# Kernel optimization log

Hardware: AMD Instinct MI355X
Metric: run time of the kernel (lower is better)

## Reference

```python
import jax, jax.numpy as jnp
import numpy as np

B, N, DIM, NUM_NODE = 512, 64, 128, 43098
ALPHA = 0.2          # LeakyReLU negative slope (opt.alpha)
NEG_INF = -9e15      # mask value used by LocalAggregator


def setup_inputs() -> dict:
    key = jax.random.key(0)
    ks = jax.random.split(key, 6)
    stdv = 1.0 / np.sqrt(DIM)
    inputs = jax.random.randint(ks[0], (B, N), 0, NUM_NODE)
    adj = jax.random.randint(ks[1], (B, N, N), 0, 5)          # edge types 0..4
    mask_item = jax.random.randint(ks[2], (B, N), 0, 2)
    item = jax.random.randint(ks[3], (B, N), 0, NUM_NODE)
    embedding = jax.random.uniform(ks[4], (NUM_NODE, DIM), minval=-stdv, maxval=stdv, dtype=jnp.float32)
    attn_a = jax.random.uniform(ks[5], (4, DIM), minval=-stdv, maxval=stdv, dtype=jnp.float32)  # a_0..a_3
    return dict(inputs=inputs, adj=adj, mask_item=mask_item, item=item,
                embedding=embedding, attn_a=attn_a)


def _local_agg(h, adj, attn_a):
    # GCE-GNN LocalAggregator: a_input[b,i,j,:] = h[b,i,:]*h[b,j,:];
    # e_k[b,i,j] = leakyrelu(a_input @ a_k). Computed without materializing
    # the [B,N,N,D] tensor: e_k = leakyrelu(einsum over d of h_i*h_j*a_k).
    e = jax.nn.leaky_relu(jnp.einsum('kd,bid,bjd->kbij', attn_a, h, h), ALPHA)  # [4,B,N,N]
    alpha = jnp.full(e.shape[1:], NEG_INF, dtype=e.dtype)
    for k in range(4):  # edge-type masked selection: adj==k+1 -> e_k
        alpha = jnp.where(adj == k + 1, e[k], alpha)
    alpha = jax.nn.softmax(alpha, axis=-1)          # [B,N,N]
    return jnp.einsum('bij,bjd->bid', alpha, h)     # [B,N,D]


def reference(inputs, adj, mask_item, item, embedding, attn_a):
    h = embedding[inputs]                 # [B,N,D] embedding gather
    h_local = _local_agg(h, adj, attn_a)  # GAT-style local aggregation
    # F.dropout with training=False (eval/inference) is identity
    return h_local
```

## Files before the change

### kernel.cpp

```cpp
#include <hip/hip_runtime.h>
#include <hip/hip_bf16.h>


#define LRELU    0.2f

typedef __bf16 bf16x8 __attribute__((ext_vector_type(8)));
typedef float  f32x4  __attribute__((ext_vector_type(4)));

union FragU { bf16x8 v; unsigned u[4]; uint4 q; };

__device__ __forceinline__ unsigned pk2(float lo, float hi) {
  __hip_bfloat162 t = __float22bfloat162_rn(float2{lo, hi});
  unsigned u;
  __builtin_memcpy(&u, &t, 4);
  return u;
}
__device__ __forceinline__ float bflo(unsigned u) { return __builtin_bit_cast(float, u << 16); }
__device__ __forceinline__ float bfhi(unsigned u) { return __builtin_bit_cast(float, u & 0xffff0000u); }

__global__ __launch_bounds__(512, 4)
void cg_kernel(const int* __restrict__ inputs, const int* __restrict__ adj,
               const float* __restrict__ embedding, const float* __restrict__ attn_a,
               float* __restrict__ out) {
  __shared__ unsigned short Hb[64 * 128];
  __shared__ unsigned short HbT[128 * 64];
  __shared__ unsigned short Pl[64 * 64];
  __shared__ float aaL[512];
  __shared__ float redS[64 * 2];

  const int b   = blockIdx.x;
  const int tid = threadIdx.x;
  const int w   = tid >> 6;
  const int l   = tid & 63;
  const int lr  = l & 15;
  const int lg  = l >> 4;
  const int it  = w >> 1;
  const int jh  = w & 1;

  char* HbB  = (char*)Hb;
  char* HbTB = (char*)HbT;
  char* PlB  = (char*)Pl;

  const int row = tid >> 3;
  const int c   = tid & 7;
  const int idx = inputs[b * 64 + row];

  int adjv[2][4];
#pragma unroll
  for (int jt2 = 0; jt2 < 2; ++jt2)
#pragma unroll
    for (int r = 0; r < 4; ++r)
      adjv[jt2][r] = adj[b * 4096 + (16 * it + 4 * lg + r) * 64 + 32 * jh + 16 * jt2 + lr];

  const float4* src = (const float4*)(embedding + (long)idx * 128 + c * 16);
  float4 v0 = src[0], v1 = src[1], v2 = src[2], v3 = src[3];
  aaL[tid] = attn_a[tid];

  unsigned pk[8];
  pk[0] = pk2(v0.x, v0.y); pk[1] = pk2(v0.z, v0.w);
  pk[2] = pk2(v1.x, v1.y); pk[3] = pk2(v1.z, v1.w);
  pk[4] = pk2(v2.x, v2.y); pk[5] = pk2(v2.z, v2.w);
  pk[6] = pk2(v3.x, v3.y); pk[7] = pk2(v3.z, v3.w);
  const int rswz = (row & 7) << 4;
  *(uint4*)(HbB + ((row * 256 + c * 32)      ^ rswz)) = uint4{pk[0], pk[1], pk[2], pk[3]};
  *(uint4*)(HbB + ((row * 256 + c * 32 + 16) ^ rswz)) = uint4{pk[4], pk[5], pk[6], pk[7]};
#pragma unroll
  for (int s = 0; s < 16; ++s) {
    int e = (s + 3 * c) & 15;
    int d = c * 16 + e;
    unsigned short hv = (unsigned short)((e & 1) ? (pk[e >> 1] >> 16) : (pk[e >> 1] & 0xffffu));
    *(unsigned short*)(HbTB + ((d * 128 + row * 2) ^ ((d & 7) << 4))) = hv;
  }
  __syncthreads();

  f32x4 acc[4][2];
#pragma unroll
  for (int k = 0; k < 4; ++k)
#pragma unroll
    for (int jt2 = 0; jt2 < 2; ++jt2) acc[k][jt2] = f32x4{0.f, 0.f, 0.f, 0.f};

  const int arow = 16 * it + lr;
  const int aswz = (lr & 7) << 4;

#pragma unroll
  for (int kc = 0; kc < 4; ++kc) {
    const int dsl = kc * 32 + lg * 8;
    uint4 ha = *(const uint4*)(HbB + ((arow * 256 + dsl * 2) ^ aswz));
    float hfa[8];
    hfa[0] = bflo(ha.x); hfa[1] = bfhi(ha.x);
    hfa[2] = bflo(ha.y); hfa[3] = bfhi(ha.y);
    hfa[4] = bflo(ha.z); hfa[5] = bfhi(ha.z);
    hfa[6] = bflo(ha.w); hfa[7] = bfhi(ha.w);
    FragU bf0, bf1;
    {
      int jr0 = 16 * (2 * jh) + lr;
      int jr1 = 16 * (2 * jh + 1) + lr;
      bf0.q = *(const uint4*)(HbB + ((jr0 * 256 + dsl * 2) ^ aswz));
      bf1.q = *(const uint4*)(HbB + ((jr1 * 256 + dsl * 2) ^ aswz));
    }
#pragma unroll
    for (int k = 0; k < 4; ++k) {
      float4 a0 = *(const float4*)&aaL[k * 128 + dsl];
      float4 a1 = *(const float4*)&aaL[k * 128 + dsl + 4];
      FragU afr;
      afr.u[0] = pk2(hfa[0] * a0.x, hfa[1] * a0.y);
      afr.u[1] = pk2(hfa[2] * a0.z, hfa[3] * a0.w);
      afr.u[2] = pk2(hfa[4] * a1.x, hfa[5] * a1.y);
      afr.u[3] = pk2(hfa[6] * a1.z, hfa[7] * a1.w);
      acc[k][0] = __builtin_amdgcn_mfma_f32_16x16x32_bf16(afr.v, bf0.v, acc[k][0], 0, 0, 0);
      acc[k][1] = __builtin_amdgcn_mfma_f32_16x16x32_bf16(afr.v, bf1.v, acc[k][1], 0, 0, 0);
    }
  }

  float p[2][4];
#pragma unroll
  for (int jt2 = 0; jt2 < 2; ++jt2)
#pragma unroll
    for (int r = 0; r < 4; ++r) {
      int av = adjv[jt2][r];
      float s = acc[0][jt2][r];
      s = (av == 2) ? acc[1][jt2][r] : s;
      s = (av == 3) ? acc[2][jt2][r] : s;
      s = (av == 4) ? acc[3][jt2][r] : s;
      float sl = s > 0.f ? s : LRELU * s;
      p[jt2][r] = (av != 0) ? __expf(sl) : 0.f;
    }
#pragma unroll
  for (int r = 0; r < 4; ++r) {
    int i = 16 * it + 4 * lg + r;
    int iswz = (i & 7) << 4;
    *(unsigned short*)(PlB + ((i * 128 + (32 * jh + lr) * 2)      ^ iswz)) = (unsigned short)(pk2(p[0][r], p[0][r]) & 0xffffu);
    *(unsigned short*)(PlB + ((i * 128 + (32 * jh + 16 + lr) * 2) ^ iswz)) = (unsigned short)(pk2(p[1][r], p[1][r]) & 0xffffu);
    float ss = p[0][r] + p[1][r];
    ss += __shfl_xor(ss, 1);
    ss += __shfl_xor(ss, 2);
    ss += __shfl_xor(ss, 4);
    ss += __shfl_xor(ss, 8);
    if (lr == 0) redS[i * 2 + jh] = ss;
  }
  __syncthreads();
  float z4[4];
#pragma unroll
  for (int r = 0; r < 4; ++r) {
    int i = 16 * it + 4 * lg + r;
    z4[r] = redS[i * 2] + redS[i * 2 + 1];
  }

  FragU afrP[2];
#pragma unroll
  for (int kc2 = 0; kc2 < 2; ++kc2) {
    int prow = 16 * it + lr;
    afrP[kc2].q = *(const uint4*)(PlB + ((prow * 128 + (kc2 * 32 + lg * 8) * 2) ^ aswz));
  }
  f32x4 pv[4];
#pragma unroll
  for (int dtl = 0; dtl < 4; ++dtl) pv[dtl] = f32x4{0.f, 0.f, 0.f, 0.f};
#pragma unroll
  for (int dtl = 0; dtl < 4; ++dtl) {
#pragma unroll
    for (int kc2 = 0; kc2 < 2; ++kc2) {
      int drow = 64 * jh + 16 * dtl + lr;
      FragU bfr;
      bfr.q = *(const uint4*)(HbTB + ((drow * 128 + (kc2 * 32 + lg * 8) * 2) ^ ((drow & 7) << 4)));
      pv[dtl] = __builtin_amdgcn_mfma_f32_16x16x32_bf16(afrP[kc2].v, bfr.v, pv[dtl], 0, 0, 0);
    }
  }

#pragma unroll
  for (int r = 0; r < 4; ++r) {
    int i = 16 * it + 4 * lg + r;
    float invz = 1.0f / z4[r];
#pragma unroll
    for (int dtl = 0; dtl < 4; ++dtl) {
      int d = 64 * jh + 16 * dtl + lr;
      out[(b * 64 + i) * 128 + d] = pv[dtl][r] * invz;
    }
  }
}

extern "C" void kernel_launch(void* const* d_in, const int* in_sizes, int n_in,
                              void* d_out, int out_size, void* d_ws, size_t ws_size,
                              hipStream_t stream) {
  (void)in_sizes; (void)n_in; (void)d_ws; (void)ws_size; (void)out_size;
  const int*   inputs    = (const int*)d_in[0];
  const int*   adj       = (const int*)d_in[1];
  const float* embedding = (const float*)d_in[4];
  const float* attn_a    = (const float*)d_in[5];
  float*       out       = (float*)d_out;
  cg_kernel<<<dim3(512), dim3(512), 0, stream>>>(inputs, adj, embedding, attn_a, out);
}
```

Baseline: 18.72 us.

## Split each batch across two 256-thread blocks by query-row halves

Each batch is now handled by two blocks of 256 threads, and each block computes 32 of the 64 query rows. Both blocks still gather and convert the full 64x128 embedding tile, plus its transpose, into shared memory, so that gather work is done twice. The aim is to double the grid to 1024 blocks for better occupancy and load balance across CUs, and to shrink per-block shared memory for the P and reduction buffers. The cost is redundant embedding loads and transposes, and more work per thread during staging.

```diff
diff --git a/kernel.cpp b/kernel.cpp
--- a/kernel.cpp
+++ b/kernel.cpp
@@ -18,17 +18,19 @@
 __device__ __forceinline__ float bflo(unsigned u) { return __builtin_bit_cast(float, u << 16); }
 __device__ __forceinline__ float bfhi(unsigned u) { return __builtin_bit_cast(float, u & 0xffff0000u); }
 
-__global__ __launch_bounds__(512, 4)
+__global__ __launch_bounds__(256, 4)
 void cg_kernel(const int* __restrict__ inputs, const int* __restrict__ adj,
                const float* __restrict__ embedding, const float* __restrict__ attn_a,
                float* __restrict__ out) {
   __shared__ unsigned short Hb[64 * 128];
   __shared__ unsigned short HbT[128 * 64];
-  __shared__ unsigned short Pl[64 * 64];
+  __shared__ unsigned short Pl[32 * 64];
   __shared__ float aaL[512];
-  __shared__ float redS[64 * 2];
-
-  const int b   = blockIdx.x;
+  __shared__ float redS[32 * 2];
+
+  const int bid = blockIdx.x;
+  const int b   = bid >> 1;
+  const int bi  = bid & 1;
   const int tid = threadIdx.x;
   const int w   = tid >> 6;
   const int l   = tid & 63;
@@ -41,33 +43,42 @@
   char* HbTB = (char*)HbT;
   char* PlB  = (char*)Pl;
 
-  const int row = tid >> 3;
-  const int c   = tid & 7;
+  const int row = tid >> 2;
+  const int c   = tid & 3;
   const int idx = inputs[b * 64 + row];
 
   int adjv[2][4];
 #pragma unroll
   for (int jt2 = 0; jt2 < 2; ++jt2)
 #pragma unroll
-    for (int r = 0; r < 4; ++r)
-      adjv[jt2][r] = adj[b * 4096 + (16 * it + 4 * lg + r) * 64 + 32 * jh + 16 * jt2 + lr];
-
-  const float4* src = (const float4*)(embedding + (long)idx * 128 + c * 16);
-  float4 v0 = src[0], v1 = src[1], v2 = src[2], v3 = src[3];
+    for (int r = 0; r < 4; ++r) {
+      int iloc = 16 * it + 4 * lg + r;
+      adjv[jt2][r] = adj[b * 4096 + (32 * bi + iloc) * 64 + 32 * jh + 16 * jt2 + lr];
+    }
+
+  const float4* src = (const float4*)(embedding + (long)idx * 128 + c * 32);
+  float4 v[8];
+#pragma unroll
+  for (int q = 0; q < 8; ++q) v[q] = src[q];
   aaL[tid] = attn_a[tid];
-
-  unsigned pk[8];
-  pk[0] = pk2(v0.x, v0.y); pk[1] = pk2(v0.z, v0.w);
-  pk[2] = pk2(v1.x, v1.y); pk[3] = pk2(v1.z, v1.w);
-  pk[4] = pk2(v2.x, v2.y); pk[5] = pk2(v2.z, v2.w);
-  pk[6] = pk2(v3.x, v3.y); pk[7] = pk2(v3.z, v3.w);
+  aaL[tid + 256] = attn_a[tid + 256];
+
+  unsigned pk[16];
+#pragma unroll
+  for (int q = 0; q < 8; ++q) {
+    pk[2 * q]     = pk2(v[q].x, v[q].y);
+    pk[2 * q + 1] = pk2(v[q].z, v[q].w);
+  }
   const int rswz = (row & 7) << 4;
-  *(uint4*)(HbB + ((row * 256 + c * 32)      ^ rswz)) = uint4{pk[0], pk[1], pk[2], pk[3]};
-  *(uint4*)(HbB + ((row * 256 + c * 32 + 16) ^ rswz)) = uint4{pk[4], pk[5], pk[6], pk[7]};
-#pragma unroll
-  for (int s = 0; s < 16; ++s) {
-    int e = (s + 3 * c) & 15;
-    int d = c * 16 + e;
+  const int base = row * 256 + c * 64;
+  *(uint4*)(HbB + ((base)      ^ rswz)) = uint4{pk[0],  pk[1],  pk[2],  pk[3]};
+  *(uint4*)(HbB + ((base + 16) ^ rswz)) = uint4{pk[4],  pk[5],  pk[6],  pk[7]};
+  *(uint4*)(HbB + ((base + 32) ^ rswz)) = uint4{pk[8],  pk[9],  pk[10], pk[11]};
+  *(uint4*)(HbB + ((base + 48) ^ rswz)) = uint4{pk[12], pk[13], pk[14], pk[15]};
+#pragma unroll
+  for (int s = 0; s < 32; ++s) {
+    int e = (s + 2 * c) & 31;
+    int d = c * 32 + e;
     unsigned short hv = (unsigned short)((e & 1) ? (pk[e >> 1] >> 16) : (pk[e >> 1] & 0xffffu));
     *(unsigned short*)(HbTB + ((d * 128 + row * 2) ^ ((d & 7) << 4))) = hv;
   }
@@ -79,7 +90,7 @@
 #pragma unroll
     for (int jt2 = 0; jt2 < 2; ++jt2) acc[k][jt2] = f32x4{0.f, 0.f, 0.f, 0.f};
 
-  const int arow = 16 * it + lr;
+  const int arow = 32 * bi + 16 * it + lr;
   const int aswz = (lr & 7) << 4;
 
 #pragma unroll
@@ -93,8 +104,8 @@
     hfa[6] = bflo(ha.w); hfa[7] = bfhi(ha.w);
     FragU bf0, bf1;
     {
-      int jr0 = 16 * (2 * jh) + lr;
-      int jr1 = 16 * (2 * jh + 1) + lr;
+      int jr0 = 32 * jh + lr;
+      int jr1 = 32 * jh + 16 + lr;
       bf0.q = *(const uint4*)(HbB + ((jr0 * 256 + dsl * 2) ^ aswz));
       bf1.q = *(const uint4*)(HbB + ((jr1 * 256 + dsl * 2) ^ aswz));
     }
@@ -127,23 +138,23 @@
     }
 #pragma unroll
   for (int r = 0; r < 4; ++r) {
-    int i = 16 * it + 4 * lg + r;
-    int iswz = (i & 7) << 4;
-    *(unsigned short*)(PlB + ((i * 128 + (32 * jh + lr) * 2)      ^ iswz)) = (unsigned short)(pk2(p[0][r], p[0][r]) & 0xffffu);
-    *(unsigned short*)(PlB + ((i * 128 + (32 * jh + 16 + lr) * 2) ^ iswz)) = (unsigned short)(pk2(p[1][r], p[1][r]) & 0xffffu);
+    int iloc = 16 * it + 4 * lg + r;
+    int iswz = (iloc & 7) << 4;
+    *(unsigned short*)(PlB + ((iloc * 128 + (32 * jh + lr) * 2)      ^ iswz)) = (unsigned short)(pk2(p[0][r], p[0][r]) & 0xffffu);
+    *(unsigned short*)(PlB + ((iloc * 128 + (32 * jh + 16 + lr) * 2) ^ iswz)) = (unsigned short)(pk2(p[1][r], p[1][r]) & 0xffffu);
     float ss = p[0][r] + p[1][r];
     ss += __shfl_xor(ss, 1);
     ss += __shfl_xor(ss, 2);
     ss += __shfl_xor(ss, 4);
     ss += __shfl_xor(ss, 8);
-    if (lr == 0) redS[i * 2 + jh] = ss;
+    if (lr == 0) redS[iloc * 2 + jh] = ss;
   }
   __syncthreads();
   float z4[4];
 #pragma unroll
   for (int r = 0; r < 4; ++r) {
-    int i = 16 * it + 4 * lg + r;
-    z4[r] = redS[i * 2] + redS[i * 2 + 1];
+    int iloc = 16 * it + 4 * lg + r;
+    z4[r] = redS[iloc * 2] + redS[iloc * 2 + 1];
   }
 
   FragU afrP[2];
@@ -168,12 +179,12 @@
 
 #pragma unroll
   for (int r = 0; r < 4; ++r) {
-    int i = 16 * it + 4 * lg + r;
+    int iloc = 16 * it + 4 * lg + r;
     float invz = 1.0f / z4[r];
 #pragma unroll
     for (int dtl = 0; dtl < 4; ++dtl) {
       int d = 64 * jh + 16 * dtl + lr;
-      out[(b * 64 + i) * 128 + d] = pv[dtl][r] * invz;
+      out[(b * 64 + 32 * bi + iloc) * 128 + d] = pv[dtl][r] * invz;
     }
   }
 }
@@ -187,5 +198,5 @@
   const float* embedding = (const float*)d_in[4];
   const float* attn_a    = (const float*)d_in[5];
   float*       out       = (float*)d_out;
-  cg_kernel<<<dim3(512), dim3(512), 0, stream>>>(inputs, adj, embedding, attn_a, out);
+  cg_kernel<<<dim3(1024), dim3(256), 0, stream>>>(inputs, adj, embedding, attn_a, out);
 }
```

New measurement: 25.05 us. 1.34x slower.

## Process two batches per block and prefetch the second batch's gather during compute

Applied to the files above, without the earlier changes.

Each block now handles two batch elements. The embedding gather and adjacency loads for the second batch are issued before computing the first, so their global-memory latency overlaps the first batch's MFMA work. The grid is halved to 256 blocks and the launch bound occupancy hint drops to 2. On a 256-CU device this leaves roughly one block per CU and serializes two batches per block, so overlap gains may be offset by lost parallelism and higher register pressure.

```diff
diff --git a/kernel.cpp b/kernel.cpp
--- a/kernel.cpp
+++ b/kernel.cpp
@@ -18,7 +18,7 @@
 __device__ __forceinline__ float bflo(unsigned u) { return __builtin_bit_cast(float, u << 16); }
 __device__ __forceinline__ float bfhi(unsigned u) { return __builtin_bit_cast(float, u & 0xffff0000u); }
 
-__global__ __launch_bounds__(512, 4)
+__global__ __launch_bounds__(512, 2)
 void cg_kernel(const int* __restrict__ inputs, const int* __restrict__ adj,
                const float* __restrict__ embedding, const float* __restrict__ attn_a,
                float* __restrict__ out) {
@@ -28,7 +28,7 @@
   __shared__ float aaL[512];
   __shared__ float redS[64 * 2];
 
-  const int b   = blockIdx.x;
+  const int bid = blockIdx.x;
   const int tid = threadIdx.x;
   const int w   = tid >> 6;
   const int l   = tid & 63;
@@ -41,141 +41,167 @@
   char* HbTB = (char*)HbT;
   char* PlB  = (char*)Pl;
 
-  const int row = tid >> 3;
-  const int c   = tid & 7;
-  const int idx = inputs[b * 64 + row];
-
-  int adjv[2][4];
+  const int row  = tid >> 3;
+  const int c    = tid & 7;
+  const int rswz = (row & 7) << 4;
+  const int aswz = (lr & 7) << 4;
+
+  aaL[tid] = attn_a[tid];
+
+  auto stage = [&](const float4& v0, const float4& v1, const float4& v2, const float4& v3) {
+    unsigned pk[8];
+    pk[0] = pk2(v0.x, v0.y); pk[1] = pk2(v0.z, v0.w);
+    pk[2] = pk2(v1.x, v1.y); pk[3] = pk2(v1.z, v1.w);
+    pk[4] = pk2(v2.x, v2.y); pk[5] = pk2(v2.z, v2.w);
+    pk[6] = pk2(v3.x, v3.y); pk[7] = pk2(v3.z, v3.w);
+    *(uint4*)(HbB + ((row * 256 + c * 32)      ^ rswz)) = uint4{pk[0], pk[1], pk[2], pk[3]};
+    *(uint4*)(HbB + ((row * 256 + c * 32 + 16) ^ rswz)) = uint4{pk[4], pk[5], pk[6], pk[7]};
+#pragma unroll
+    for (int s = 0; s < 16; ++s) {
+      int e = (s + 3 * c) & 15;
+      int d = c * 16 + e;
+      unsigned short hv = (unsigned short)((e & 1) ? (pk[e >> 1] >> 16) : (pk[e >> 1] & 0xffffu));
+      *(unsigned short*)(HbTB + ((d * 128 + row * 2) ^ ((d & 7) << 4))) = hv;
+    }
+  };
+
+  auto compute = [&](int b, const int (&adjv)[2][4]) {
+    f32x4 acc[4][2];
+#pragma unroll
+    for (int k = 0; k < 4; ++k)
+#pragma unroll
+      for (int jt2 = 0; jt2 < 2; ++jt2) acc[k][jt2] = f32x4{0.f, 0.f, 0.f, 0.f};
+
+    const int arow = 16 * it + lr;
+#pragma unroll
+    for (int kc = 0; kc < 4; ++kc) {
+      const int dsl = kc * 32 + lg * 8;
+      uint4 ha = *(const uint4*)(HbB + ((arow * 256 + dsl * 2) ^ aswz));
+      float hfa[8];
+      hfa[0] = bflo(ha.x); hfa[1] = bfhi(ha.x);
+      hfa[2] = bflo(ha.y); hfa[3] = bfhi(ha.y);
+      hfa[4] = bflo(ha.z); hfa[5] = bfhi(ha.z);
+      hfa[6] = bflo(ha.w); hfa[7] = bfhi(ha.w);
+      FragU bf0, bf1;
+      {
+        int jr0 = 32 * jh + lr;
+        int jr1 = 32 * jh + 16 + lr;
+        bf0.q = *(const uint4*)(HbB + ((jr0 * 256 + dsl * 2) ^ aswz));
+        bf1.q = *(const uint4*)(HbB + ((jr1 * 256 + dsl * 2) ^ aswz));
+      }
+#pragma unroll
+      for (int k = 0; k < 4; ++k) {
+        float4 a0 = *(const float4*)&aaL[k * 128 + dsl];
+        float4 a1 = *(const float4*)&aaL[k * 128 + dsl + 4];
+        FragU afr;
+        afr.u[0] = pk2(hfa[0] * a0.x, hfa[1] * a0.y);
+        afr.u[1] = pk2(hfa[2] * a0.z, hfa[3] * a0.w);
+        afr.u[2] = pk2(hfa[4] * a1.x, hfa[5] * a1.y);
+        afr.u[3] = pk2(hfa[6] * a1.z, hfa[7] * a1.w);
+        acc[k][0] = __builtin_amdgcn_mfma_f32_16x16x32_bf16(afr.v, bf0.v, acc[k][0], 0, 0, 0);
+        acc[k][1] = __builtin_amdgcn_mfma_f32_16x16x32_bf16(afr.v, bf1.v, acc[k][1], 0, 0, 0);
+      }
+    }
+
+    float p[2][4];
+#pragma unroll
+    for (int jt2 = 0; jt2 < 2; ++jt2)
+#pragma unroll
+      for (int r = 0; r < 4; ++r) {
+        int av = adjv[jt2][r];
+        float s = acc[0][jt2][r];
+        s = (av == 2) ? acc[1][jt2][r] : s;
+        s = (av == 3) ? acc[2][jt2][r] : s;
+        s = (av == 4) ? acc[3][jt2][r] : s;
+        float sl = s > 0.f ? s : LRELU * s;
+        p[jt2][r] = (av != 0) ? __expf(sl) : 0.f;
+      }
+#pragma unroll
+    for (int r = 0; r < 4; ++r) {
+      int i = 16 * it + 4 * lg + r;
+      int iswz = (i & 7) << 4;
+      *(unsigned short*)(PlB + ((i * 128 + (32 * jh + lr) * 2)      ^ iswz)) = (unsigned short)(pk2(p[0][r], p[0][r]) & 0xffffu);
+      *(unsigned short*)(PlB + ((i * 128 + (32 * jh + 16 + lr) * 2) ^ iswz)) = (unsigned short)(pk2(p[1][r], p[1][r]) & 0xffffu);
+      float ss = p[0][r] + p[1][r];
+      ss += __shfl_xor(ss, 1);
+      ss += __shfl_xor(ss, 2);
+      ss += __shfl_xor(ss, 4);
+      ss += __shfl_xor(ss, 8);
+      if (lr == 0) redS[i * 2 + jh] = ss;
+    }
+    __syncthreads();
+    float z4[4];
+#pragma unroll
+    for (int r = 0; r < 4; ++r) {
+      int i = 16 * it + 4 * lg + r;
+      z4[r] = redS[i * 2] + redS[i * 2 + 1];
+    }
+
+    FragU afrP[2];
+#pragma unroll
+    for (int kc2 = 0; kc2 < 2; ++kc2) {
+      int prow = 16 * it + lr;
+      afrP[kc2].q = *(const uint4*)(PlB + ((prow * 128 + (kc2 * 32 + lg * 8) * 2) ^ aswz));
+    }
+    f32x4 pv[4];
+#pragma unroll
+    for (int dtl = 0; dtl < 4; ++dtl) pv[dtl] = f32x4{0.f, 0.f, 0.f, 0.f};
+#pragma unroll
+    for (int dtl = 0; dtl < 4; ++dtl) {
+#pragma unroll
+      for (int kc2 = 0; kc2 < 2; ++kc2) {
+        int drow = 64 * jh + 16 * dtl + lr;
+        FragU bfr;
+        bfr.q = *(const uint4*)(HbTB + ((drow * 128 + (kc2 * 32 + lg * 8) * 2) ^ ((drow & 7) << 4)));
+        pv[dtl] = __builtin_amdgcn_mfma_f32_16x16x32_bf16(afrP[kc2].v, bfr.v, pv[dtl], 0, 0, 0);
+      }
+    }
+#pragma unroll
+    for (int r = 0; r < 4; ++r) {
+      int i = 16 * it + 4 * lg + r;
+      float invz = 1.0f / z4[r];
+#pragma unroll
+      for (int dtl = 0; dtl < 4; ++dtl) {
+        int d = 64 * jh + 16 * dtl + lr;
+        out[(b * 64 + i) * 128 + d] = pv[dtl][r] * invz;
+      }
+    }
+  };
+
+  const int bA = 2 * bid;
+  const int bB = 2 * bid + 1;
+
+  int adjA[2][4];
 #pragma unroll
   for (int jt2 = 0; jt2 < 2; ++jt2)
 #pragma unroll
     for (int r = 0; r < 4; ++r)
-      adjv[jt2][r] = adj[b * 4096 + (16 * it + 4 * lg + r) * 64 + 32 * jh + 16 * jt2 + lr];
-
-  const float4* src = (const float4*)(embedding + (long)idx * 128 + c * 16);
-  float4 v0 = src[0], v1 = src[1], v2 = src[2], v3 = src[3];
-  aaL[tid] = attn_a[tid];
-
-  unsigned pk[8];
-  pk[0] = pk2(v0.x, v0.y); pk[1] = pk2(v0.z, v0.w);
-  pk[2] = pk2(v1.x, v1.y); pk[3] = pk2(v1.z, v1.w);
-  pk[4] = pk2(v2.x, v2.y); pk[5] = pk2(v2.z, v2.w);
-  pk[6] = pk2(v3.x, v3.y); pk[7] = pk2(v3.z, v3.w);
-  const int rswz = (row & 7) << 4;
-  *(uint4*)(HbB + ((row * 256 + c * 32)      ^ rswz)) = uint4{pk[0], pk[1], pk[2], pk[3]};
-  *(uint4*)(HbB + ((row * 256 + c * 32 + 16) ^ rswz)) = uint4{pk[4], pk[5], pk[6], pk[7]};
-#pragma unroll
-  for (int s = 0; s < 16; ++s) {
-    int e = (s + 3 * c) & 15;
-    int d = c * 16 + e;
-    unsigned short hv = (unsigned short)((e & 1) ? (pk[e >> 1] >> 16) : (pk[e >> 1] & 0xffffu));
-    *(unsigned short*)(HbTB + ((d * 128 + row * 2) ^ ((d & 7) << 4))) = hv;
+      adjA[jt2][r] = adj[bA * 4096 + (16 * it + 4 * lg + r) * 64 + 32 * jh + 16 * jt2 + lr];
+  {
+    const int idxA = inputs[bA * 64 + row];
+    const float4* srcA = (const float4*)(embedding + (long)idxA * 128 + c * 16);
+    float4 a0 = srcA[0], a1 = srcA[1], a2 = srcA[2], a3 = srcA[3];
+    stage(a0, a1, a2, a3);
   }
   __syncthreads();
 
-  f32x4 acc[4][2];
-#pragma unroll
-  for (int k = 0; k < 4; ++k)
-#pragma unroll
-    for (int jt2 = 0; jt2 < 2; ++jt2) acc[k][jt2] = f32x4{0.f, 0.f, 0.f, 0.f};
-
-  const int arow = 16 * it + lr;
-  const int aswz = (lr & 7) << 4;
-
-#pragma unroll
-  for (int kc = 0; kc < 4; ++kc) {
-    const int dsl = kc * 32 + lg * 8;
-    uint4 ha = *(const uint4*)(HbB + ((arow * 256 + dsl * 2) ^ aswz));
-    float hfa[8];
-    hfa[0] = bflo(ha.x); hfa[1] = bfhi(ha.x);
-    hfa[2] = bflo(ha.y); hfa[3] = bfhi(ha.y);
-    hfa[4] = bflo(ha.z); hfa[5] = bfhi(ha.z);
-    hfa[6] = bflo(ha.w); hfa[7] = bfhi(ha.w);
-    FragU bf0, bf1;
-    {
-      int jr0 = 16 * (2 * jh) + lr;
-      int jr1 = 16 * (2 * jh + 1) + lr;
-      bf0.q = *(const uint4*)(HbB + ((jr0 * 256 + dsl * 2) ^ aswz));
-      bf1.q = *(const uint4*)(HbB + ((jr1 * 256 + dsl * 2) ^ aswz));
-    }
-#pragma unroll
-    for (int k = 0; k < 4; ++k) {
-      float4 a0 = *(const float4*)&aaL[k * 128 + dsl];
-      float4 a1 = *(const float4*)&aaL[k * 128 + dsl + 4];
-      FragU afr;
-      afr.u[0] = pk2(hfa[0] * a0.x, hfa[1] * a0.y);
-      afr.u[1] = pk2(hfa[2] * a0.z, hfa[3] * a0.w);
-      afr.u[2] = pk2(hfa[4] * a1.x, hfa[5] * a1.y);
-      afr.u[3] = pk2(hfa[6] * a1.z, hfa[7] * a1.w);
-      acc[k][0] = __builtin_amdgcn_mfma_f32_16x16x32_bf16(afr.v, bf0.v, acc[k][0], 0, 0, 0);
-      acc[k][1] = __builtin_amdgcn_mfma_f32_16x16x32_bf16(afr.v, bf1.v, acc[k][1], 0, 0, 0);
-    }
-  }
-
-  float p[2][4];
+  const int idxB = inputs[bB * 64 + row];
+  const float4* srcB = (const float4*)(embedding + (long)idxB * 128 + c * 16);
+  float4 b0 = srcB[0], b1 = srcB[1], b2 = srcB[2], b3 = srcB[3];
+  int adjB[2][4];
 #pragma unroll
   for (int jt2 = 0; jt2 < 2; ++jt2)
 #pragma unroll
-    for (int r = 0; r < 4; ++r) {
-      int av = adjv[jt2][r];
-      float s = acc[0][jt2][r];
-      s = (av == 2) ? acc[1][jt2][r] : s;
-      s = (av == 3) ? acc[2][jt2][r] : s;
-      s = (av == 4) ? acc[3][jt2][r] : s;
-      float sl = s > 0.f ? s : LRELU * s;
-      p[jt2][r] = (av != 0) ? __expf(sl) : 0.f;
-    }
-#pragma unroll
-  for (int r = 0; r < 4; ++r) {
-    int i = 16 * it + 4 * lg + r;
-    int iswz = (i & 7) << 4;
-    *(unsigned short*)(PlB + ((i * 128 + (32 * jh + lr) * 2)      ^ iswz)) = (unsigned short)(pk2(p[0][r], p[0][r]) & 0xffffu);
-    *(unsigned short*)(PlB + ((i * 128 + (32 * jh + 16 + lr) * 2) ^ iswz)) = (unsigned short)(pk2(p[1][r], p[1][r]) & 0xffffu);
-    float ss = p[0][r] + p[1][r];
-    ss += __shfl_xor(ss, 1);
-    ss += __shfl_xor(ss, 2);
-    ss += __shfl_xor(ss, 4);
-    ss += __shfl_xor(ss, 8);
-    if (lr == 0) redS[i * 2 + jh] = ss;
-  }
+    for (int r = 0; r < 4; ++r)
+      adjB[jt2][r] = adj[bB * 4096 + (16 * it + 4 * lg + r) * 64 + 32 * jh + 16 * jt2 + lr];
+
+  compute(bA, adjA);
+
   __syncthreads();
-  float z4[4];
-#pragma unroll
-  for (int r = 0; r < 4; ++r) {
-    int i = 16 * it + 4 * lg + r;
-    z4[r] = redS[i * 2] + redS[i * 2 + 1];
-  }
-
-  FragU afrP[2];
-#pragma unroll
-  for (int kc2 = 0; kc2 < 2; ++kc2) {
-    int prow = 16 * it + lr;
-    afrP[kc2].q = *(const uint4*)(PlB + ((prow * 128 + (kc2 * 32 + lg * 8) * 2) ^ aswz));
-  }
-  f32x4 pv[4];
-#pragma unroll
-  for (int dtl = 0; dtl < 4; ++dtl) pv[dtl] = f32x4{0.f, 0.f, 0.f, 0.f};
-#pragma unroll
-  for (int dtl = 0; dtl < 4; ++dtl) {
-#pragma unroll
-    for (int kc2 = 0; kc2 < 2; ++kc2) {
-      int drow = 64 * jh + 16 * dtl + lr;
-      FragU bfr;
-      bfr.q = *(const uint4*)(HbTB + ((drow * 128 + (kc2 * 32 + lg * 8) * 2) ^ ((drow & 7) << 4)));
-      pv[dtl] = __builtin_amdgcn_mfma_f32_16x16x32_bf16(afrP[kc2].v, bfr.v, pv[dtl], 0, 0, 0);
-    }
-  }
-
-#pragma unroll
-  for (int r = 0; r < 4; ++r) {
-    int i = 16 * it + 4 * lg + r;
-    float invz = 1.0f / z4[r];
-#pragma unroll
-    for (int dtl = 0; dtl < 4; ++dtl) {
-      int d = 64 * jh + 16 * dtl + lr;
-      out[(b * 64 + i) * 128 + d] = pv[dtl][r] * invz;
-    }
-  }
+  stage(b0, b1, b2, b3);
+  __syncthreads();
+
+  compute(bB, adjB);
 }
 
 extern "C" void kernel_launch(void* const* d_in, const int* in_sizes, int n_in,
@@ -187,5 +213,5 @@
   const float* embedding = (const float*)d_in[4];
   const float* attn_a    = (const float*)d_in[5];
   float*       out       = (float*)d_out;
-  cg_kernel<<<dim3(512), dim3(512), 0, stream>>>(inputs, adj, embedding, attn_a, out);
+  cg_kernel<<<dim3(256), dim3(512), 0, stream>>>(inputs, adj, embedding, attn_a, out);
 }
```

After: 19.57 us. +4.6%, slower.
